# Performance work log

Measured on AMD Instinct MI355X. Metric: run time of the kernel, lower is better.

The kernel has to match this reference:

```python
import jax, jax.numpy as jnp
import numpy as np

D_MODEL = 2048
NUM_EXPERTS = 128
TOP_K = 8
NORM_P = 2.0  # normalize_expert_weights


def setup_inputs() -> dict:
    key = jax.random.key(0)
    k1, k2 = jax.random.split(key)
    x = jax.random.normal(k1, (4, 4096, D_MODEL), dtype=jnp.float32)
    # router weight ~ trunc_normal(std=0.02); plain normal*0.02 is fine for a numeric baseline
    weight = jax.random.normal(k2, (NUM_EXPERTS, D_MODEL), dtype=jnp.float32) * 0.02
    score_bias = jnp.zeros((NUM_EXPERTS,), dtype=jnp.float32)
    return {"x": x, "weight": weight, "score_bias": score_bias}


def reference(x, weight, score_bias):
    # Flatten tokens: (B, S, D) -> (N, D); router always runs in fp32 (x.float())
    B, S, D = x.shape
    xf = x.reshape(B * S, D).astype(jnp.float32)
    # get_expert_logits: F.linear(x, weight.view(E, D)) -> (N, E)
    logits = jnp.einsum("nd,ed->ne", xf, weight.astype(jnp.float32))
    # softmax gating
    scores = jax.nn.softmax(logits, axis=-1)
    # bias-adjusted top-k (bias only affects selection, not the returned weights)
    biased = scores + score_bias[None, :]
    _, expert_indices = jax.lax.top_k(biased, TOP_K)          # (N, top_k)
    expert_weights = jnp.take_along_axis(scores, expert_indices, axis=-1)
    # normalize_expert_weights = 2.0 -> divide by L2 norm across top_k
    norm = jnp.linalg.norm(expert_weights, ord=NORM_P, axis=-1, keepdims=True)
    expert_weights = expert_weights / norm
    return expert_weights, expert_indices
```

## Files before the change

kernel.cpp:

```cpp
#include <hip/hip_runtime.h>
#include <hip/hip_bf16.h>
#include <math.h>


#define NE     128
#define TOKT   128
#define KC     32
#define KS     4
#define DMODEL 2048
#define DSLICE (DMODEL / KS)

typedef __attribute__((ext_vector_type(8))) short short8;
typedef __attribute__((ext_vector_type(4))) float f32x4;

union S8 { short s[8]; short8 v; };

__device__ __forceinline__ void split3(float f, S8& hi, S8& mi, S8& lo, int j) {
  const unsigned u0 = __float_as_uint(f);
  const float hif = __uint_as_float(u0 & 0xFFFF0000u);
  const float r1 = f - hif;
  const unsigned u1 = __float_as_uint(r1);
  const float mif = __uint_as_float(u1 & 0xFFFF0000u);
  const float r2 = r1 - mif;
  hi.s[j] = (short)(u0 >> 16);
  mi.s[j] = (short)(u1 >> 16);
  lo.s[j] = (short)(__float_as_uint(r2) >> 16);
}

__global__ __launch_bounds__(256) void logits_mfma(
    const float* __restrict__ x, const float* __restrict__ w,
    float* __restrict__ part, int N) {
  __shared__ short xs[3][TOKT][KC];
  __shared__ short wsm[3][NE][KC];

  const int tid  = threadIdx.x;
  const int wave = tid >> 6;
  const int lane = tid & 63;
  const int wm = wave >> 1;
  const int wn = wave & 1;
  const int quad = lane >> 4;
  const int l16  = lane & 15;
  const size_t tokBase = (size_t)blockIdx.x * TOKT;
  const int d0 = blockIdx.y * DSLICE;

  const int r = tid >> 1;
  const int h = tid & 1;

  f32x4 acc[4][4];
#pragma unroll
  for (int i = 0; i < 4; ++i)
#pragma unroll
    for (int j = 0; j < 4; ++j) acc[i][j] = (f32x4)(0.f);

  for (int kc = 0; kc < DSLICE; kc += KC) {
    __syncthreads();
    {
      const float* gx = x + (tokBase + r) * DMODEL + d0 + kc + h * 16;
      const float* gw = w + (size_t)r * DMODEL + d0 + kc + h * 16;
#pragma unroll
      for (int run = 0; run < 2; ++run) {
        const float4 a0 = *(const float4*)(gx + run * 8);
        const float4 a1 = *(const float4*)(gx + run * 8 + 4);
        S8 hi, mi, lo;
        split3(a0.x, hi, mi, lo, 0); split3(a0.y, hi, mi, lo, 1);
        split3(a0.z, hi, mi, lo, 2); split3(a0.w, hi, mi, lo, 3);
        split3(a1.x, hi, mi, lo, 4); split3(a1.y, hi, mi, lo, 5);
        split3(a1.z, hi, mi, lo, 6); split3(a1.w, hi, mi, lo, 7);
        const int kk = h * 16 + run * 8;
        *(short8*)&xs[0][r][kk] = hi.v;
        *(short8*)&xs[1][r][kk] = mi.v;
        *(short8*)&xs[2][r][kk] = lo.v;
        const float4 b0 = *(const float4*)(gw + run * 8);
        const float4 b1 = *(const float4*)(gw + run * 8 + 4);
        split3(b0.x, hi, mi, lo, 0); split3(b0.y, hi, mi, lo, 1);
        split3(b0.z, hi, mi, lo, 2); split3(b0.w, hi, mi, lo, 3);
        split3(b1.x, hi, mi, lo, 4); split3(b1.y, hi, mi, lo, 5);
        split3(b1.z, hi, mi, lo, 6); split3(b1.w, hi, mi, lo, 7);
        *(short8*)&wsm[0][r][kk] = hi.v;
        *(short8*)&wsm[1][r][kk] = mi.v;
        *(short8*)&wsm[2][r][kk] = lo.v;
      }
    }
    __syncthreads();

    short8 af[4][3];
#pragma unroll
    for (int mt = 0; mt < 4; ++mt)
#pragma unroll
      for (int p = 0; p < 3; ++p)
        af[mt][p] = *(const short8*)&xs[p][wm * 64 + mt * 16 + l16][quad * 8];

#pragma unroll
    for (int nt = 0; nt < 4; ++nt) {
      short8 bf[3];
#pragma unroll
      for (int p = 0; p < 3; ++p)
        bf[p] = *(const short8*)&wsm[p][wn * 64 + nt * 16 + l16][quad * 8];
#pragma unroll
      for (int mt = 0; mt < 4; ++mt) {
        f32x4 c = acc[mt][nt];
        c = __builtin_amdgcn_mfma_f32_16x16x32_bf16(af[mt][0], bf[0], c, 0, 0, 0);
        c = __builtin_amdgcn_mfma_f32_16x16x32_bf16(af[mt][0], bf[1], c, 0, 0, 0);
        c = __builtin_amdgcn_mfma_f32_16x16x32_bf16(af[mt][1], bf[0], c, 0, 0, 0);
        c = __builtin_amdgcn_mfma_f32_16x16x32_bf16(af[mt][0], bf[2], c, 0, 0, 0);
        c = __builtin_amdgcn_mfma_f32_16x16x32_bf16(af[mt][2], bf[0], c, 0, 0, 0);
        c = __builtin_amdgcn_mfma_f32_16x16x32_bf16(af[mt][1], bf[1], c, 0, 0, 0);
        acc[mt][nt] = c;
      }
    }
  }

#pragma unroll
  for (int mt = 0; mt < 4; ++mt)
#pragma unroll
    for (int nt = 0; nt < 4; ++nt) {
      const int ex = wn * 64 + nt * 16 + l16;
#pragma unroll
      for (int reg = 0; reg < 4; ++reg) {
        const size_t tok = tokBase + wm * 64 + mt * 16 + quad * 4 + reg;
        part[((size_t)blockIdx.y * N + tok) * NE + ex] = acc[mt][nt][reg];
      }
    }
}

__global__ __launch_bounds__(256) void router_topk(
    const float* __restrict__ part, const float* __restrict__ bias,
    float* __restrict__ outW, float* __restrict__ outI, int ks, int N) {
  const int wave = threadIdx.x >> 6;
  const int lane = threadIdx.x & 63;
  const int token = blockIdx.x * 4 + wave;
  if (token >= N) return;

  float l0 = 0.f, l1 = 0.f;
  for (int k = 0; k < ks; ++k) {
    const float* p = part + ((size_t)k * N + token) * NE;
    l0 += p[lane];
    l1 += p[lane + 64];
  }

  float m = fmaxf(l0, l1);
#pragma unroll
  for (int off = 1; off < 64; off <<= 1) m = fmaxf(m, __shfl_xor(m, off));
  const float ev0 = __expf(l0 - m);
  const float ev1 = __expf(l1 - m);
  float zs = ev0 + ev1;
#pragma unroll
  for (int off = 1; off < 64; off <<= 1) zs += __shfl_xor(zs, off);
  const float s0 = ev0 / zs;
  const float s1 = ev1 / zs;

  float b0 = s0 + bias[lane];
  float b1 = s1 + bias[lane + 64];

  float myv = 0.f;
  int myi = 0;
  float ss = 0.f;
#pragma unroll
  for (int rnd = 0; rnd < 8; ++rnd) {
    float key; int idx;
    if (b0 >= b1) { key = b0; idx = lane; }
    else          { key = b1; idx = lane + 64; }
#pragma unroll
    for (int off = 1; off < 64; off <<= 1) {
      const float k2 = __shfl_xor(key, off);
      const int   i2 = __shfl_xor(idx, off);
      if (k2 > key || (k2 == key && i2 < idx)) { key = k2; idx = i2; }
    }
    const float cand = (idx < 64) ? s0 : s1;
    const float sw = __shfl(cand, idx & 63);
    ss = fmaf(sw, sw, ss);
    if (lane == rnd) { myv = sw; myi = idx; }
    if (lane == (idx & 63)) { if (idx < 64) b0 = -INFINITY; else b1 = -INFINITY; }
  }

  const float inv = 1.f / sqrtf(ss);
  if (lane < 8) {
    outW[(size_t)token * 8 + lane] = myv * inv;
    outI[(size_t)token * 8 + lane] = (float)myi;
  }
}

extern "C" void kernel_launch(void* const* d_in, const int* in_sizes, int n_in,
                              void* d_out, int out_size, void* d_ws, size_t ws_size,
                              hipStream_t stream) {
  const float* x    = (const float*)d_in[0];
  const float* w    = (const float*)d_in[1];
  const float* bias = (const float*)d_in[2];
  float* out = (float*)d_out;

  const int N = in_sizes[0] / DMODEL;
  float* part = (float*)d_ws;

  logits_mfma<<<dim3(N / TOKT, KS), 256, 0, stream>>>(x, w, part, N);
  router_topk<<<(N + 3) / 4, 256, 0, stream>>>(part, bias, out, out + (size_t)N * 8, KS, N);
}
```

Measured before the change: 224.2 us.

## Prefetch next K-chunk into registers and pad LDS rows against bank conflicts

Global loads for the next K chunk of x and w are issued into registers before the MFMA loop of the current chunk. This lets memory latency overlap with compute instead of stalling at the start of each iteration. The LDS rows are also padded from 32 to 40 shorts, which removes bank conflicts on the short8 fragment reads. The cost is more live registers, which may lower occupancy, and slightly more shared memory.

Result: no change. 227.0 us (+1.2%).

```diff
diff --git a/kernel.cpp b/kernel.cpp
--- a/kernel.cpp
+++ b/kernel.cpp
@@ -6,6 +6,7 @@
 #define NE     128
 #define TOKT   128
 #define KC     32
+#define KROW   40
 #define KS     4
 #define DMODEL 2048
 #define DSLICE (DMODEL / KS)
@@ -27,11 +28,19 @@
   lo.s[j] = (short)(__float_as_uint(r2) >> 16);
 }
 
+__device__ __forceinline__ void split8(const float4& a0, const float4& a1,
+                                       S8& hi, S8& mi, S8& lo) {
+  split3(a0.x, hi, mi, lo, 0); split3(a0.y, hi, mi, lo, 1);
+  split3(a0.z, hi, mi, lo, 2); split3(a0.w, hi, mi, lo, 3);
+  split3(a1.x, hi, mi, lo, 4); split3(a1.y, hi, mi, lo, 5);
+  split3(a1.z, hi, mi, lo, 6); split3(a1.w, hi, mi, lo, 7);
+}
+
 __global__ __launch_bounds__(256) void logits_mfma(
     const float* __restrict__ x, const float* __restrict__ w,
     float* __restrict__ part, int N) {
-  __shared__ short xs[3][TOKT][KC];
-  __shared__ short wsm[3][NE][KC];
+  __shared__ short xs[3][TOKT * KROW];
+  __shared__ short wsm[3][NE * KROW];
 
   const int tid  = threadIdx.x;
   const int wave = tid >> 6;
@@ -46,40 +55,57 @@
   const int r = tid >> 1;
   const int h = tid & 1;
 
+  const float* gx = x + (tokBase + r) * DMODEL + d0 + h * 16;
+  const float* gw = w + (size_t)r * DMODEL + d0 + h * 16;
+
   f32x4 acc[4][4];
 #pragma unroll
   for (int i = 0; i < 4; ++i)
 #pragma unroll
     for (int j = 0; j < 4; ++j) acc[i][j] = (f32x4)(0.f);
+
+  float4 px0 = *(const float4*)(gx + 0);
+  float4 px1 = *(const float4*)(gx + 4);
+  float4 px2 = *(const float4*)(gx + 8);
+  float4 px3 = *(const float4*)(gx + 12);
+  float4 pw0 = *(const float4*)(gw + 0);
+  float4 pw1 = *(const float4*)(gw + 4);
+  float4 pw2 = *(const float4*)(gw + 8);
+  float4 pw3 = *(const float4*)(gw + 12);
 
   for (int kc = 0; kc < DSLICE; kc += KC) {
     __syncthreads();
     {
-      const float* gx = x + (tokBase + r) * DMODEL + d0 + kc + h * 16;
-      const float* gw = w + (size_t)r * DMODEL + d0 + kc + h * 16;
-#pragma unroll
-      for (int run = 0; run < 2; ++run) {
-        const float4 a0 = *(const float4*)(gx + run * 8);
-        const float4 a1 = *(const float4*)(gx + run * 8 + 4);
-        S8 hi, mi, lo;
-        split3(a0.x, hi, mi, lo, 0); split3(a0.y, hi, mi, lo, 1);
-        split3(a0.z, hi, mi, lo, 2); split3(a0.w, hi, mi, lo, 3);
-        split3(a1.x, hi, mi, lo, 4); split3(a1.y, hi, mi, lo, 5);
-        split3(a1.z, hi, mi, lo, 6); split3(a1.w, hi, mi, lo, 7);
-        const int kk = h * 16 + run * 8;
-        *(short8*)&xs[0][r][kk] = hi.v;
-        *(short8*)&xs[1][r][kk] = mi.v;
-        *(short8*)&xs[2][r][kk] = lo.v;
-        const float4 b0 = *(const float4*)(gw + run * 8);
-        const float4 b1 = *(const float4*)(gw + run * 8 + 4);
-        split3(b0.x, hi, mi, lo, 0); split3(b0.y, hi, mi, lo, 1);
-        split3(b0.z, hi, mi, lo, 2); split3(b0.w, hi, mi, lo, 3);
-        split3(b1.x, hi, mi, lo, 4); split3(b1.y, hi, mi, lo, 5);
-        split3(b1.z, hi, mi, lo, 6); split3(b1.w, hi, mi, lo, 7);
-        *(short8*)&wsm[0][r][kk] = hi.v;
-        *(short8*)&wsm[1][r][kk] = mi.v;
-        *(short8*)&wsm[2][r][kk] = lo.v;
-      }
+      S8 hi, mi, lo;
+      const int kk0 = h * 16;
+      split8(px0, px1, hi, mi, lo);
+      *(short8*)&xs[0][r * KROW + kk0] = hi.v;
+      *(short8*)&xs[1][r * KROW + kk0] = mi.v;
+      *(short8*)&xs[2][r * KROW + kk0] = lo.v;
+      split8(px2, px3, hi, mi, lo);
+      *(short8*)&xs[0][r * KROW + kk0 + 8] = hi.v;
+      *(short8*)&xs[1][r * KROW + kk0 + 8] = mi.v;
+      *(short8*)&xs[2][r * KROW + kk0 + 8] = lo.v;
+      split8(pw0, pw1, hi, mi, lo);
+      *(short8*)&wsm[0][r * KROW + kk0] = hi.v;
+      *(short8*)&wsm[1][r * KROW + kk0] = mi.v;
+      *(short8*)&wsm[2][r * KROW + kk0] = lo.v;
+      split8(pw2, pw3, hi, mi, lo);
+      *(short8*)&wsm[0][r * KROW + kk0 + 8] = hi.v;
+      *(short8*)&wsm[1][r * KROW + kk0 + 8] = mi.v;
+      *(short8*)&wsm[2][r * KROW + kk0 + 8] = lo.v;
+    }
+    if (kc + KC < DSLICE) {
+      const float* nx = gx + kc + KC;
+      const float* nw = gw + kc + KC;
+      px0 = *(const float4*)(nx + 0);
+      px1 = *(const float4*)(nx + 4);
+      px2 = *(const float4*)(nx + 8);
+      px3 = *(const float4*)(nx + 12);
+      pw0 = *(const float4*)(nw + 0);
+      pw1 = *(const float4*)(nw + 4);
+      pw2 = *(const float4*)(nw + 8);
+      pw3 = *(const float4*)(nw + 12);
     }
     __syncthreads();
 
@@ -88,14 +114,14 @@
     for (int mt = 0; mt < 4; ++mt)
 #pragma unroll
       for (int p = 0; p < 3; ++p)
-        af[mt][p] = *(const short8*)&xs[p][wm * 64 + mt * 16 + l16][quad * 8];
+        af[mt][p] = *(const short8*)&xs[p][(wm * 64 + mt * 16 + l16) * KROW + quad * 8];
 
 #pragma unroll
     for (int nt = 0; nt < 4; ++nt) {
       short8 bf[3];
 #pragma unroll
       for (int p = 0; p < 3; ++p)
-        bf[p] = *(const short8*)&wsm[p][wn * 64 + nt * 16 + l16][quad * 8];
+        bf[p] = *(const short8*)&wsm[p][(wn * 64 + nt * 16 + l16) * KROW + quad * 8];
 #pragma unroll
       for (int mt = 0; mt < 4; ++mt) {
         f32x4 c = acc[mt][nt];
```
